# Performance work log

Hardware: AMD Instinct MI355X
Metric: run time of the kernel (lower is better)

The kernel has to match this reference:

```python
import jax, jax.numpy as jnp
import numpy as np

H = 64          # nhid
L = 2           # nlayer
N_LEFT = 100000
N_RIGHT = 100000
E = 1000000
EPS = 1e-5

PNAMES = ["nn1_w1", "nn1_b1", "nn1_w2", "nn1_b2",
          "nn2_w1", "nn2_b1", "nn2_w2", "nn2_b2",
          "l1_w", "l1_b", "l2_w", "l2_b", "l3_w", "l3_b", "l4_w", "l4_b",
          "out_w1", "out_b1", "out_w2", "out_b2"]


def _bn_relu(x):
    # BatchNorm1d (training-mode batch stats, affine=False / default-init affine) + ReLU
    m = x.mean(0, keepdims=True)
    v = jnp.mean((x - m) ** 2, axis=0, keepdims=True)  # biased var, as torch BN
    return jax.nn.relu((x - m) * jax.lax.rsqrt(v + EPS))


def _mlp2(x, w1, b1, w2, b2):
    # MLP(nin, nout, nlayer=2, with_final_activation=True): (Linear->BN->ReLU) x2
    h = _bn_relu(x @ w1 + b1)
    return _bn_relu(h @ w2 + b2)


def _lin_bn_relu(x, w, b):
    # nn.Linear -> BatchNorm1d(affine=False) -> ReLU
    return _bn_relu(x @ w + b)


def _gscatter(msg, idx, n):
    # generalized_scatter with aggregators ['add','mean','max'], concatenated
    s = jax.ops.segment_sum(msg, idx, num_segments=n)
    cnt = jax.ops.segment_sum(jnp.ones((msg.shape[0],), msg.dtype), idx, num_segments=n)[:, None]
    mean = s / jnp.maximum(cnt, 1.0)
    mx = jax.ops.segment_max(msg, idx, num_segments=n)
    mx = jnp.where(cnt > 0, mx, 0.0)  # empty segments -> 0
    return jnp.concatenate([s, mean, mx], axis=-1)  # [n, 3*d]


def _parallel_layer(xs, src, dst, nl, p):
    # nl = n_left (static). combined_batch = [0]*nl + [1]*nr (sorted), last = 1.
    nr = xs.shape[0] - nl
    x_right = xs[nl:]                                   # batch != 0
    right_info = _gscatter(x_right[dst], src, nl)       # [nl, 3H]
    x_left_new = _mlp2(xs, p["nn1_w1"], p["nn1_b1"], p["nn1_w2"], p["nn1_b2"])[:nl]
    left_info = _gscatter(x_left_new[src], dst, nr)     # [nr, 3H]
    right_info_new = _mlp2(right_info, p["nn2_w1"], p["nn2_b1"], p["nn2_w2"], p["nn2_b2"])
    right_left_info = _gscatter(right_info_new[src], dst, nr)  # [nr, 3H]
    x = _lin_bn_relu(xs, p["l1_w"], p["l1_b"])                 # [N, H//2]
    ri = _lin_bn_relu(right_info, p["l2_w"], p["l2_b"])        # [nl, H//2]
    li = _lin_bn_relu(left_info, p["l3_w"], p["l3_b"])         # [nr, H//2]
    rli = _lin_bn_relu(right_left_info, p["l4_w"], p["l4_b"])  # [nr, H//2]
    # clone-and-masked-assign patterns become static-slice concatenations
    right_full = jnp.concatenate([ri, x[nl:]], axis=0)   # rows batch!=last <- ri
    left_full = jnp.concatenate([x[:nl], li], axis=0)    # rows batch!=0    <- li
    rl_full = jnp.concatenate([x[:nl], rli], axis=0)
    h = jnp.concatenate([x, right_full, left_full, rl_full], axis=-1)  # [N, 2H]
    return _mlp2(h, p["out_w1"], p["out_b1"], p["out_w2"], p["out_b2"])


def _forward(xs, params, src, dst, n_left):
    for l in range(L):
        p = {name: params[name][l] for name in PNAMES}
        xs = xs + _parallel_layer(xs, src, dst, n_left, p)  # residual; dropout=0, eval
    return xs  # output_encoder is Identity (nin == nout)


def setup_inputs() -> dict:
    key = jax.random.key(0)
    ks = iter(jax.random.split(key, 40))
    def w(shape, s=0.1):
        return jax.random.normal(next(ks), shape, jnp.float32) * s
    inp = {
        "xs": jax.random.normal(next(ks), (N_LEFT + N_RIGHT, H), jnp.float32),
        "nn1_w1": w((L, H, H)), "nn1_b1": w((L, H)),
        "nn1_w2": w((L, H, H)), "nn1_b2": w((L, H)),
        "nn2_w1": w((L, 3 * H, H)), "nn2_b1": w((L, H)),
        "nn2_w2": w((L, H, H)), "nn2_b2": w((L, H)),
        "l1_w": w((L, H, H // 2)), "l1_b": w((L, H // 2)),
        "l2_w": w((L, 3 * H, H // 2)), "l2_b": w((L, H // 2)),
        "l3_w": w((L, 3 * H, H // 2)), "l3_b": w((L, H // 2)),
        "l4_w": w((L, 3 * H, H // 2)), "l4_b": w((L, H // 2)),
        "out_w1": w((L, 2 * H, H)), "out_b1": w((L, H)),
        "out_w2": w((L, H, H)), "out_b2": w((L, H)),
        "src": jax.random.randint(next(ks), (E,), 0, N_LEFT),
        "dst": jax.random.randint(next(ks), (E,), 0, N_RIGHT),
        "n_left": N_LEFT,
    }
    return inp


def reference(xs, nn1_w1, nn1_b1, nn1_w2, nn1_b2, nn2_w1, nn2_b1, nn2_w2, nn2_b2,
              l1_w, l1_b, l2_w, l2_b, l3_w, l3_b, l4_w, l4_b,
              out_w1, out_b1, out_w2, out_b2, src, dst, n_left):
    params = dict(zip(PNAMES, (nn1_w1, nn1_b1, nn1_w2, nn1_b2,
                               nn2_w1, nn2_b1, nn2_w2, nn2_b2,
                               l1_w, l1_b, l2_w, l2_b, l3_w, l3_b, l4_w, l4_b,
                               out_w1, out_b1, out_w2, out_b2)))
    return _forward(xs, params, src, dst, int(n_left))
```

## Files before the change

kernel.cpp:

```cpp
#include <hip/hip_runtime.h>

#define NLEFT  100000
#define NRIGHT 100000
#define NTOT   200000
#define NEDGE  1000000
#define HD     64
#define BNEPS  1e-5f

typedef __attribute__((ext_vector_type(8))) short bfrag8;
typedef __attribute__((ext_vector_type(4))) float facc4;

__device__ inline unsigned short f2bf(float f) {
  unsigned u = __float_as_uint(f);
  u = u + 0x7fffu + ((u >> 16) & 1u);
  return (unsigned short)(u >> 16);
}
__device__ inline float bf2f(unsigned short u) {
  return __uint_as_float((unsigned)u << 16);
}

#define WC_G1    0
#define WC_G2    18432
#define WC_G3    24576
#define WC_NN2W2 30720
#define WC_M2    34816
#define WC_NN1W2 40960
#define WC_OUTW1 45056
#define WC_OUTW2 53248
#define WC_PER_L 57344


__global__ __launch_bounds__(256) void init_kernel(const float* __restrict__ xs,
                                                   float* __restrict__ out,
                                                   unsigned short* __restrict__ outbf,
                                                   float* __restrict__ st, int nst,
                                                   int* __restrict__ cl, int* __restrict__ cr,
                                                   int* __restrict__ curl, int* __restrict__ curr) {
  size_t ng = (size_t)NTOT * HD / 4;
  for (size_t i = (size_t)blockIdx.x * blockDim.x + threadIdx.x; i < ng;
       i += (size_t)gridDim.x * blockDim.x) {
    float4 v = reinterpret_cast<const float4*>(xs)[i];
    reinterpret_cast<float4*>(out)[i] = v;
    ushort4 p;
    p.x = f2bf(v.x); p.y = f2bf(v.y); p.z = f2bf(v.z); p.w = f2bf(v.w);
    reinterpret_cast<ushort4*>(outbf)[i] = p;
  }
  for (int i = blockIdx.x * blockDim.x + threadIdx.x; i < NLEFT;
       i += gridDim.x * blockDim.x) {
    cl[i] = 0; curl[i] = 0; cr[i] = 0; curr[i] = 0;
    if (i < nst) st[i] = 0.f;
  }
}

__global__ __launch_bounds__(256) void count_kernel(const int* __restrict__ src,
                                                    const int* __restrict__ dst,
                                                    int* __restrict__ cl, int* __restrict__ cr) {
  for (int e = blockIdx.x * blockDim.x + threadIdx.x; e < NEDGE;
       e += gridDim.x * blockDim.x) {
    atomicAdd(&cl[src[e]], 1);
    atomicAdd(&cr[dst[e]], 1);
  }
}


__global__ __launch_bounds__(256) void wconv_kernel(const float* __restrict__ l2w,
                                                    const float* __restrict__ nn2w1,
                                                    const float* __restrict__ l4w,
                                                    const float* __restrict__ l3w,
                                                    const float* __restrict__ nn2w2,
                                                    const float* __restrict__ nn1w1,
                                                    const float* __restrict__ l1w,
                                                    const float* __restrict__ nn1w2,
                                                    const float* __restrict__ outw1,
                                                    const float* __restrict__ outw2,
                                                    unsigned short* __restrict__ dst) {
  for (int idx = blockIdx.x * 256 + threadIdx.x; idx < 2 * WC_PER_L;
       idx += gridDim.x * 256) {
    int l = idx / WC_PER_L;
    int r = idx - l * WC_PER_L;
    const float* src; int N, n, k;
    if (r < WC_G2) {
      n = r / 192; k = r - n * 192;
      if (n < 32) { src = l2w + (size_t)l * 192 * 32; N = 32; }
      else        { src = nn2w1 + (size_t)l * 192 * 64; N = 64; n -= 32; }
    } else if (r < WC_G3) {
      int rr = r - WC_G2; n = rr / 192; k = rr - n * 192;
      src = l4w + (size_t)l * 192 * 32; N = 32;
    } else if (r < WC_NN2W2) {
      int rr = r - WC_G3; n = rr / 192; k = rr - n * 192;
      src = l3w + (size_t)l * 192 * 32; N = 32;
    } else if (r < WC_M2) {
      int rr = r - WC_NN2W2; n = rr / 64; k = rr - n * 64;
      src = nn2w2 + (size_t)l * 64 * 64; N = 64;
    } else if (r < WC_NN1W2) {
      int rr = r - WC_M2; n = rr / 64; k = rr - n * 64;
      if (n < 64) { src = nn1w1 + (size_t)l * 64 * 64; N = 64; }
      else        { src = l1w + (size_t)l * 64 * 32; N = 32; n -= 64; }
    } else if (r < WC_OUTW1) {
      int rr = r - WC_NN1W2; n = rr / 64; k = rr - n * 64;
      src = nn1w2 + (size_t)l * 64 * 64; N = 64;
    } else if (r < WC_OUTW2) {
      int rr = r - WC_OUTW1; n = rr / 128; k = rr - n * 128;
      src = outw1 + (size_t)l * 128 * 64; N = 64;
    } else {
      int rr = r - WC_OUTW2; n = rr / 64; k = rr - n * 64;
      src = outw2 + (size_t)l * 64 * 64; N = 64;
    }
    dst[idx] = f2bf(src[(size_t)k * N + n]);
  }
}


__global__ __launch_bounds__(256) void scan1_kernel(const int* __restrict__ cnt, int n,
                                                    int* __restrict__ partial) {
  __shared__ int tmp[256];
  int i = blockIdx.x * 256 + threadIdx.x;
  tmp[threadIdx.x] = (i < n) ? cnt[i] : 0;
  __syncthreads();
  for (int s = 128; s > 0; s >>= 1) {
    if (threadIdx.x < s) tmp[threadIdx.x] += tmp[threadIdx.x + s];
    __syncthreads();
  }
  if (threadIdx.x == 0) partial[blockIdx.x] = tmp[0];
}

__global__ __launch_bounds__(1024) void scan2_kernel(int* __restrict__ partial, int nb) {
  __shared__ int tmp[1024];
  int t = threadIdx.x;
  int v = (t < nb) ? partial[t] : 0;
  tmp[t] = v;
  __syncthreads();
  for (int off = 1; off < 1024; off <<= 1) {
    int x = tmp[t];
    int add = (t >= off) ? tmp[t - off] : 0;
    __syncthreads();
    tmp[t] = x + add;
    __syncthreads();
  }
  if (t < nb) partial[t] = tmp[t] - v;
}

__global__ __launch_bounds__(256) void scan3_kernel(const int* __restrict__ cnt, int n,
                                                    const int* __restrict__ partial,
                                                    int* __restrict__ offs) {
  __shared__ int tmp[256];
  int t = threadIdx.x;
  int i = blockIdx.x * 256 + t;
  int v = (i < n) ? cnt[i] : 0;
  tmp[t] = v;
  __syncthreads();
  for (int off = 1; off < 256; off <<= 1) {
    int x = tmp[t];
    int add = (t >= off) ? tmp[t - off] : 0;
    __syncthreads();
    tmp[t] = x + add;
    __syncthreads();
  }
  if (i < n) offs[i] = tmp[t] - v + partial[blockIdx.x];
  if (i == 0) offs[n] = NEDGE;
}


__global__ __launch_bounds__(256) void fill_kernel(const int* __restrict__ src,
                                                   const int* __restrict__ dst,
                                                   const int* __restrict__ oL,
                                                   const int* __restrict__ oR,
                                                   int* __restrict__ curL, int* __restrict__ curR,
                                                   int* __restrict__ adjL, int* __restrict__ adjR) {
  for (int e = blockIdx.x * blockDim.x + threadIdx.x; e < NEDGE;
       e += gridDim.x * blockDim.x) {
    int s = src[e], d = dst[e];
    int p = atomicAdd(&curL[s], 1);
    adjL[oL[s] + p] = d;
    int q = atomicAdd(&curR[d], 1);
    adjR[oR[d] + q] = s;
  }
}


template <int N1, int N2, bool SRCNORM>
__global__ __launch_bounds__(512) void gmm_mfma(const unsigned short* __restrict__ mat,
                                                const int* __restrict__ offs,
                                                const int* __restrict__ adj,
                                                int nseg,
                                                const float* __restrict__ st_src, float inv_src,
                                                const unsigned short* __restrict__ Wbf,
                                                const float* __restrict__ B1,
                                                unsigned short* __restrict__ Y1,
                                                float* __restrict__ st1,
                                                const float* __restrict__ B2,
                                                unsigned short* __restrict__ Y2,
                                                float* __restrict__ st2) {
  constexpr int K    = 192;
  constexpr int LDX  = 200;
  constexpr int SEGS = 32;
  constexpr int NT   = N1 + N2;
  constexpr int CTT  = NT / 16;
  constexpr int CTW  = (CTT >= 6) ? 2 : 1;
  constexpr int NGRP = CTT / CTW;
  constexpr int NWM  = 2 * NGRP;
  __shared__ alignas(16) unsigned short xl[SEGS * LDX];
  __shared__ alignas(16) unsigned short wl[NT * LDX];
  __shared__ float bl[NT];
  __shared__ float ldsS[NT], ldsQ[NT];

  int tid = threadIdx.x;
  for (int i = tid; i < NT * 24; i += 512) {
    int n = i / 24, kk = (i - n * 24) * 8;
    *reinterpret_cast<bfrag8*>(&wl[n * LDX + kk]) =
        *reinterpret_cast<const bfrag8*>(&Wbf[n * 192 + kk]);
  }
  for (int i = tid; i < N1; i += 512) bl[i] = B1[i];
  if constexpr (N2 > 0)
    for (int i = tid; i < N2; i += 512) bl[N1 + i] = B2[i];
  if (tid < NT) { ldsS[tid] = 0.f; ldsQ[tid] = 0.f; }

  int wave = tid >> 6;
  int lane = tid & 63;
  int half = lane >> 5;
  int c0   = (lane & 31) * 2;

  float nm0 = 0.f, nm1 = 0.f, ns0 = 1.f, ns1 = 1.f;
  if (SRCNORM) {
    float m0 = st_src[c0] * inv_src, m1 = st_src[c0 + 1] * inv_src;
    float v0 = st_src[64 + c0] * inv_src - m0 * m0;
    float v1 = st_src[64 + c0 + 1] * inv_src - m1 * m1;
    nm0 = m0; nm1 = m1;
    ns0 = rsqrtf(fmaxf(v0, 0.f) + BNEPS);
    ns1 = rsqrtf(fmaxf(v1, 0.f) + BNEPS);
  }

  int lr  = lane & 15;
  int lk  = (lane >> 4) * 8;
  int lj4 = (lane >> 4) * 4;
  int rowtile = wave & 1;
  int colgrp  = wave >> 1;
  int rowbase = rowtile * 16;

  float sacc[CTW], qacc[CTW];
#pragma unroll
  for (int ct = 0; ct < CTW; ct++) { sacc[ct] = 0.f; qacc[ct] = 0.f; }

  int tiles = (nseg + SEGS - 1) / SEGS;
  for (int t = blockIdx.x; t < tiles; t += gridDim.x) {
    __syncthreads();
    int segbase = t * SEGS + wave * 4;
    for (int s = 0; s < 4; s++) {
      int seg = segbase + s;
      int row = wave * 4 + s;
      float s0 = 0.f, s1 = 0.f, m0 = -INFINITY, m1 = -INFINITY;
      int cdeg = 0;
      if (seg < nseg) {
        int b = offs[seg], e = offs[seg + 1];
        cdeg = e - b;
        for (int jb = b + half; jb < e; jb += 16) {
          unsigned pk[8];
#pragma unroll
          for (int u = 0; u < 8; u++) {
            int j = jb + 2 * u;
            pk[u] = 0;
            if (j < e) {
              int g = adj[j];
              pk[u] = *reinterpret_cast<const unsigned*>(&mat[(size_t)g * HD + c0]);
            }
          }
#pragma unroll
          for (int u = 0; u < 8; u++) {
            int j = jb + 2 * u;
            if (j < e) {
              float v0 = __uint_as_float(pk[u] << 16);
              float v1 = __uint_as_float(pk[u] & 0xffff0000u);
              if (SRCNORM) {
                v0 = fmaxf((v0 - nm0) * ns0, 0.f);
                v1 = fmaxf((v1 - nm1) * ns1, 0.f);
              }
              s0 += v0; s1 += v1;
              m0 = fmaxf(m0, v0); m1 = fmaxf(m1, v1);
            }
          }
        }
        s0 += __shfl_xor(s0, 32);
        s1 += __shfl_xor(s1, 32);
        m0 = fmaxf(m0, __shfl_xor(m0, 32));
        m1 = fmaxf(m1, __shfl_xor(m1, 32));
      }
      float inv = 1.f / fmaxf((float)cdeg, 1.f);
      if (cdeg == 0) { m0 = 0.f; m1 = 0.f; s0 = 0.f; s1 = 0.f; }
      if (half == 0) {
        unsigned sp = (unsigned)f2bf(s0) | ((unsigned)f2bf(s1) << 16);
        unsigned mp = (unsigned)f2bf(m0) | ((unsigned)f2bf(m1) << 16);
        *reinterpret_cast<unsigned*>(&xl[row * LDX + c0])       = sp;
        *reinterpret_cast<unsigned*>(&xl[row * LDX + 128 + c0]) = mp;
      } else {
        unsigned ap = (unsigned)f2bf(s0 * inv) | ((unsigned)f2bf(s1 * inv) << 16);
        *reinterpret_cast<unsigned*>(&xl[row * LDX + 64 + c0]) = ap;
      }
    }
    __syncthreads();

    if (wave < NWM) {
      facc4 acc[CTW];
#pragma unroll
      for (int ct = 0; ct < CTW; ct++) acc[ct] = (facc4){0.f, 0.f, 0.f, 0.f};
#pragma unroll
      for (int kt = 0; kt < K / 32; kt++) {
        bfrag8 a = *reinterpret_cast<const bfrag8*>(&xl[(rowbase + lr) * LDX + kt * 32 + lk]);
#pragma unroll
        for (int ct = 0; ct < CTW; ct++) {
          bfrag8 b = *reinterpret_cast<const bfrag8*>(
              &wl[((colgrp * CTW + ct) * 16 + lr) * LDX + kt * 32 + lk]);
          acc[ct] = __builtin_amdgcn_mfma_f32_16x16x32_bf16(a, b, acc[ct], 0, 0, 0);
        }
      }
#pragma unroll
      for (int ct = 0; ct < CTW; ct++) {
        int col = (colgrp * CTW + ct) * 16 + lr;
        float bias = bl[col];
#pragma unroll
        for (int j = 0; j < 4; j++) {
          int grow = t * SEGS + rowbase + lj4 + j;
          if (grow < nseg) {
            float v = acc[ct][j] + bias;
            if (col < N1) Y1[(size_t)grow * N1 + col] = f2bf(v);
            else          Y2[(size_t)grow * N2 + (col - N1)] = f2bf(v);
            sacc[ct] += v; qacc[ct] += v * v;
          }
        }
      }
    }
  }

  __syncthreads();
  if (wave < NWM) {
#pragma unroll
    for (int ct = 0; ct < CTW; ct++) {
      int col = (colgrp * CTW + ct) * 16 + lr;
      atomicAdd(&ldsS[col], sacc[ct]);
      atomicAdd(&ldsQ[col], qacc[ct]);
    }
  }
  __syncthreads();
  if (tid < NT) {
    if (tid < N1) {
      atomicAdd(&st1[tid], ldsS[tid]);
      atomicAdd(&st1[N1 + tid], ldsQ[tid]);
    } else {
      atomicAdd(&st2[tid - N1], ldsS[tid]);
      atomicAdd(&st2[N2 + (tid - N1)], ldsQ[tid]);
    }
  }
}


template <int K, int N, int ROWS, bool NIN>
__global__ __launch_bounds__(256) void mm_mfma(const unsigned short* __restrict__ X,
                                               const unsigned short* __restrict__ Wbf,
                                               const float* __restrict__ Bv,
                                               unsigned short* __restrict__ Y, int M,
                                               float* __restrict__ st_out,
                                               const float* __restrict__ st_in, float inv_m) {
  constexpr int LDX = K + 8;
  constexpr int RT  = ROWS / 64;
  constexpr int CT  = N / 16;
  constexpr int KV  = K / 8;
  __shared__ alignas(16) unsigned short xl[ROWS * LDX];
  __shared__ alignas(16) unsigned short wl[N * LDX];
  __shared__ float bl[N];
  __shared__ float nmean[K], nscal[K];
  __shared__ float ldsS[N], ldsQ[N];

  int tid = threadIdx.x;
  for (int i = tid; i < N * KV; i += 256) {
    int n = i / KV, kk = (i - n * KV) * 8;
    *reinterpret_cast<bfrag8*>(&wl[n * LDX + kk]) =
        *reinterpret_cast<const bfrag8*>(&Wbf[n * K + kk]);
  }
  for (int i = tid; i < N; i += 256) bl[i] = Bv[i];
  if (NIN) {
    for (int i = tid; i < K; i += 256) {
      float m = st_in[i] * inv_m;
      float v = st_in[K + i] * inv_m - m * m;
      nmean[i] = m;
      nscal[i] = rsqrtf(fmaxf(v, 0.f) + BNEPS);
    }
  }
  if (tid < N) { ldsS[tid] = 0.f; ldsQ[tid] = 0.f; }

  int lane = tid & 63;
  int wv   = tid >> 6;
  int lr   = lane & 15;
  int lk   = (lane >> 4) * 8;
  int lj4  = (lane >> 4) * 4;
  int rowbase = wv * (RT * 16);

  float sc[CT], sq[CT];
#pragma unroll
  for (int c = 0; c < CT; c++) { sc[c] = 0.f; sq[c] = 0.f; }

  int tiles = (M + ROWS - 1) / ROWS;
  for (int t = blockIdx.x; t < tiles; t += gridDim.x) {
    int r0 = t * ROWS;
    __syncthreads();
    for (int i = tid * 8; i < ROWS * K; i += 2048) {
      int r = i / K, c = i - r * K;
      int row = r0 + r;
      bfrag8 v = {0, 0, 0, 0, 0, 0, 0, 0};
      if (row < M) {
        v = *reinterpret_cast<const bfrag8*>(X + (size_t)row * K + c);
        if (NIN) {
#pragma unroll
          for (int j = 0; j < 8; j++) {
            float f = bf2f((unsigned short)v[j]);
            f = fmaxf((f - nmean[c + j]) * nscal[c + j], 0.f);
            v[j] = (short)f2bf(f);
          }
        }
      }
      *reinterpret_cast<bfrag8*>(&xl[r * LDX + c]) = v;
    }
    __syncthreads();

    facc4 acc[RT][CT];
#pragma unroll
    for (int rt = 0; rt < RT; rt++)
#pragma unroll
      for (int ct = 0; ct < CT; ct++) acc[rt][ct] = (facc4){0.f, 0.f, 0.f, 0.f};

#pragma unroll
    for (int kt = 0; kt < K / 32; kt++) {
      bfrag8 a[RT], b[CT];
#pragma unroll
      for (int rt = 0; rt < RT; rt++)
        a[rt] = *reinterpret_cast<const bfrag8*>(&xl[(rowbase + rt * 16 + lr) * LDX + kt * 32 + lk]);
#pragma unroll
      for (int ct = 0; ct < CT; ct++)
        b[ct] = *reinterpret_cast<const bfrag8*>(&wl[(ct * 16 + lr) * LDX + kt * 32 + lk]);
#pragma unroll
      for (int rt = 0; rt < RT; rt++)
#pragma unroll
        for (int ct = 0; ct < CT; ct++)
          acc[rt][ct] = __builtin_amdgcn_mfma_f32_16x16x32_bf16(a[rt], b[ct], acc[rt][ct], 0, 0, 0);
    }

#pragma unroll
    for (int rt = 0; rt < RT; rt++) {
#pragma unroll
      for (int ct = 0; ct < CT; ct++) {
        int col = ct * 16 + lr;
        float bcol = bl[col];
#pragma unroll
        for (int j = 0; j < 4; j++) {
          int row = r0 + rowbase + rt * 16 + lj4 + j;
          if (row < M) {
            float v = acc[rt][ct][j] + bcol;
            Y[(size_t)row * N + col] = f2bf(v);
            sc[ct] += v; sq[ct] += v * v;
          }
        }
      }
    }
  }

  __syncthreads();
#pragma unroll
  for (int ct = 0; ct < CT; ct++) {
    atomicAdd(&ldsS[ct * 16 + lr], sc[ct]);
    atomicAdd(&ldsQ[ct * 16 + lr], sq[ct]);
  }
  __syncthreads();
  if (tid < N) {
    atomicAdd(&st_out[tid], ldsS[tid]);
    atomicAdd(&st_out[N + tid], ldsQ[tid]);
  }
}


__global__ __launch_bounds__(256) void mm2_mfma(const unsigned short* __restrict__ X,
                                                const unsigned short* __restrict__ Wbf,
                                                const float* __restrict__ B1,
                                                unsigned short* __restrict__ Y1,
                                                float* __restrict__ st1,
                                                const float* __restrict__ B2,
                                                unsigned short* __restrict__ Y2,
                                                float* __restrict__ st2,
                                                int M) {
  constexpr int K = 64, N1 = 64, N2 = 32, NT = 96, ROWS = 128;
  constexpr int LDX = K + 8, RT = 2, CT = 6, KV = K / 8;
  __shared__ alignas(16) unsigned short xl[ROWS * LDX];
  __shared__ alignas(16) unsigned short wl[NT * LDX];
  __shared__ float bl[NT];
  __shared__ float ldsS[NT], ldsQ[NT];

  int tid = threadIdx.x;
  for (int i = tid; i < NT * KV; i += 256) {
    int n = i / KV, kk = (i - n * KV) * 8;
    *reinterpret_cast<bfrag8*>(&wl[n * LDX + kk]) =
        *reinterpret_cast<const bfrag8*>(&Wbf[n * K + kk]);
  }
  for (int i = tid; i < N1; i += 256) bl[i] = B1[i];
  for (int i = tid; i < N2; i += 256) bl[N1 + i] = B2[i];
  if (tid < NT) { ldsS[tid] = 0.f; ldsQ[tid] = 0.f; }

  int lane = tid & 63;
  int wv   = tid >> 6;
  int lr   = lane & 15;
  int lk   = (lane >> 4) * 8;
  int lj4  = (lane >> 4) * 4;
  int rowbase = wv * 32;

  float sc[CT], sq[CT];
#pragma unroll
  for (int c = 0; c < CT; c++) { sc[c] = 0.f; sq[c] = 0.f; }

  int tiles = (M + ROWS - 1) / ROWS;
  for (int t = blockIdx.x; t < tiles; t += gridDim.x) {
    int r0 = t * ROWS;
    __syncthreads();
    for (int i = tid * 8; i < ROWS * K; i += 2048) {
      int r = i / K, c = i - r * K;
      int row = r0 + r;
      bfrag8 v = {0, 0, 0, 0, 0, 0, 0, 0};
      if (row < M) v = *reinterpret_cast<const bfrag8*>(X + (size_t)row * K + c);
      *reinterpret_cast<bfrag8*>(&xl[r * LDX + c]) = v;
    }
    __syncthreads();

    facc4 acc[RT][CT];
#pragma unroll
    for (int rt = 0; rt < RT; rt++)
#pragma unroll
      for (int ct = 0; ct < CT; ct++) acc[rt][ct] = (facc4){0.f, 0.f, 0.f, 0.f};

#pragma unroll
    for (int kt = 0; kt < K / 32; kt++) {
      bfrag8 a[RT], b[CT];
#pragma unroll
      for (int rt = 0; rt < RT; rt++)
        a[rt] = *reinterpret_cast<const bfrag8*>(&xl[(rowbase + rt * 16 + lr) * LDX + kt * 32 + lk]);
#pragma unroll
      for (int ct = 0; ct < CT; ct++)
        b[ct] = *reinterpret_cast<const bfrag8*>(&wl[(ct * 16 + lr) * LDX + kt * 32 + lk]);
#pragma unroll
      for (int rt = 0; rt < RT; rt++)
#pragma unroll
        for (int ct = 0; ct < CT; ct++)
          acc[rt][ct] = __builtin_amdgcn_mfma_f32_16x16x32_bf16(a[rt], b[ct], acc[rt][ct], 0, 0, 0);
    }

#pragma unroll
    for (int rt = 0; rt < RT; rt++) {
#pragma unroll
      for (int ct = 0; ct < CT; ct++) {
        int col = ct * 16 + lr;
        float bcol = bl[col];
#pragma unroll
        for (int j = 0; j < 4; j++) {
          int row = r0 + rowbase + rt * 16 + lj4 + j;
          if (row < M) {
            float v = acc[rt][ct][j] + bcol;
            if (col < N1) Y1[(size_t)row * N1 + col] = f2bf(v);
            else          Y2[(size_t)row * N2 + (col - N1)] = f2bf(v);
            sc[ct] += v; sq[ct] += v * v;
          }
        }
      }
    }
  }

  __syncthreads();
#pragma unroll
  for (int ct = 0; ct < CT; ct++) {
    atomicAdd(&ldsS[ct * 16 + lr], sc[ct]);
    atomicAdd(&ldsQ[ct * 16 + lr], sq[ct]);
  }
  __syncthreads();
  if (tid < NT) {
    if (tid < N1) {
      atomicAdd(&st1[tid], ldsS[tid]);
      atomicAdd(&st1[N1 + tid], ldsQ[tid]);
    } else {
      atomicAdd(&st2[tid - N1], ldsS[tid]);
      atomicAdd(&st2[N2 + (tid - N1)], ldsQ[tid]);
    }
  }
}


__global__ __launch_bounds__(256) void mmh_mfma(const unsigned short* __restrict__ x32,
                                                const unsigned short* __restrict__ ri,
                                                const unsigned short* __restrict__ li,
                                                const unsigned short* __restrict__ rli,
                                                const float* __restrict__ stx,
                                                const float* __restrict__ stri,
                                                const float* __restrict__ stli,
                                                const float* __restrict__ strli,
                                                const unsigned short* __restrict__ Wbf,
                                                const float* __restrict__ Bv,
                                                unsigned short* __restrict__ Y,
                                                float* __restrict__ st_out) {
  constexpr int K = 128, N = 64, ROWS = 128, LDX = K + 8, RT = 2, CT = 4, KV = K / 8;
  __shared__ alignas(16) unsigned short xl[ROWS * LDX];
  __shared__ alignas(16) unsigned short wl[N * LDX];
  __shared__ float bl[N];
  __shared__ float m4[4 * 32], s4[4 * 32];
  __shared__ float ldsS[N], ldsQ[N];

  int tid = threadIdx.x;
  for (int i = tid; i < N * KV; i += 256) {
    int n = i / KV, kk = (i - n * KV) * 8;
    *reinterpret_cast<bfrag8*>(&wl[n * LDX + kk]) =
        *reinterpret_cast<const bfrag8*>(&Wbf[n * K + kk]);
  }
  for (int i = tid; i < N; i += 256) bl[i] = Bv[i];
  if (tid < 128) {
    int s = tid >> 5, c = tid & 31;
    const float* st = (s == 0) ? stx : (s == 1) ? stri : (s == 2) ? stli : strli;
    float inv = (s == 0) ? (1.f / NTOT) : (s == 1) ? (1.f / NLEFT) : (1.f / NRIGHT);
    float m = st[c] * inv;
    float v = st[32 + c] * inv - m * m;
    m4[tid] = m;
    s4[tid] = rsqrtf(fmaxf(v, 0.f) + BNEPS);
  }
  if (tid < N) { ldsS[tid] = 0.f; ldsQ[tid] = 0.f; }

  int lane = tid & 63;
  int wv   = tid >> 6;
  int lr   = lane & 15;
  int lk   = (lane >> 4) * 8;
  int lj4  = (lane >> 4) * 4;
  int rowbase = wv * 32;

  float sc[CT], sq[CT];
#pragma unroll
  for (int c = 0; c < CT; c++) { sc[c] = 0.f; sq[c] = 0.f; }

  const int M = NTOT;
  int tiles = (M + ROWS - 1) / ROWS;
  for (int t = blockIdx.x; t < tiles; t += gridDim.x) {
    int r0 = t * ROWS;
    __syncthreads();
    for (int i = tid * 8; i < ROWS * K; i += 2048) {
      int r = i / K, c = i - r * K;
      int row = r0 + r;
      bfrag8 v = {0, 0, 0, 0, 0, 0, 0, 0};
      if (row < M) {
        int cb = c >> 5, cc = c & 31;
        const unsigned short* srcp;
        int set, srow;
        if (row < NLEFT) {
          if (cb == 1) { srcp = ri;  set = 1; srow = row; }
          else         { srcp = x32; set = 0; srow = row; }
        } else {
          int rr = row - NLEFT;
          if (cb <= 1)      { srcp = x32; set = 0; srow = row; }
          else if (cb == 2) { srcp = li;  set = 2; srow = rr; }
          else              { srcp = rli; set = 3; srow = rr; }
        }
        v = *reinterpret_cast<const bfrag8*>(srcp + (size_t)srow * 32 + cc);
        const float* mm_ = &m4[set * 32 + cc];
        const float* ss_ = &s4[set * 32 + cc];
#pragma unroll
        for (int j = 0; j < 8; j++) {
          float f = bf2f((unsigned short)v[j]);
          f = fmaxf((f - mm_[j]) * ss_[j], 0.f);
          v[j] = (short)f2bf(f);
        }
      }
      *reinterpret_cast<bfrag8*>(&xl[r * LDX + c]) = v;
    }
    __syncthreads();

    facc4 acc[RT][CT];
#pragma unroll
    for (int rt = 0; rt < RT; rt++)
#pragma unroll
      for (int ct = 0; ct < CT; ct++) acc[rt][ct] = (facc4){0.f, 0.f, 0.f, 0.f};

#pragma unroll
    for (int kt = 0; kt < K / 32; kt++) {
      bfrag8 a[RT], b[CT];
#pragma unroll
      for (int rt = 0; rt < RT; rt++)
        a[rt] = *reinterpret_cast<const bfrag8*>(&xl[(rowbase + rt * 16 + lr) * LDX + kt * 32 + lk]);
#pragma unroll
      for (int ct = 0; ct < CT; ct++)
        b[ct] = *reinterpret_cast<const bfrag8*>(&wl[(ct * 16 + lr) * LDX + kt * 32 + lk]);
#pragma unroll
      for (int rt = 0; rt < RT; rt++)
#pragma unroll
        for (int ct = 0; ct < CT; ct++)
          acc[rt][ct] = __builtin_amdgcn_mfma_f32_16x16x32_bf16(a[rt], b[ct], acc[rt][ct], 0, 0, 0);
    }

#pragma unroll
    for (int rt = 0; rt < RT; rt++) {
#pragma unroll
      for (int ct = 0; ct < CT; ct++) {
        int col = ct * 16 + lr;
        float bcol = bl[col];
#pragma unroll
        for (int j = 0; j < 4; j++) {
          int row = r0 + rowbase + rt * 16 + lj4 + j;
          if (row < M) {
            float v = acc[rt][ct][j] + bcol;
            Y[(size_t)row * N + col] = f2bf(v);
            sc[ct] += v; sq[ct] += v * v;
          }
        }
      }
    }
  }

  __syncthreads();
#pragma unroll
  for (int ct = 0; ct < CT; ct++) {
    atomicAdd(&ldsS[ct * 16 + lr], sc[ct]);
    atomicAdd(&ldsQ[ct * 16 + lr], sq[ct]);
  }
  __syncthreads();
  if (tid < N) {
    atomicAdd(&st_out[tid], ldsS[tid]);
    atomicAdd(&st_out[N + tid], ldsQ[tid]);
  }
}


__global__ __launch_bounds__(256) void norm_add_kernel(const unsigned short* __restrict__ X, int M,
                                                       const float* __restrict__ st,
                                                       float* __restrict__ D,
                                                       unsigned short* __restrict__ Dbf) {
  __shared__ float mean[64], scal[64];
  if (threadIdx.x < 64) {
    float m = st[threadIdx.x] / (float)M;
    float v = st[64 + threadIdx.x] / (float)M - m * m;
    mean[threadIdx.x] = m;
    scal[threadIdx.x] = rsqrtf(fmaxf(v, 0.f) + BNEPS);
  }
  __syncthreads();
  size_t ngrp = (size_t)M * 64 / 8;
  for (size_t i = (size_t)blockIdx.x * 256 + threadIdx.x; i < ngrp;
       i += (size_t)gridDim.x * 256) {
    size_t base = i * 8;
    int c = (int)(base & 63);
    bfrag8 xv = *reinterpret_cast<const bfrag8*>(&X[base]);
    float4 d0 = *reinterpret_cast<float4*>(&D[base]);
    float4 d1 = *reinterpret_cast<float4*>(&D[base + 4]);
    float o[8];
#pragma unroll
    for (int j = 0; j < 8; j++) {
      float y = (bf2f((unsigned short)xv[j]) - mean[c + j]) * scal[c + j];
      y = y > 0.f ? y : 0.f;
      float dv = (j < 4) ? (&d0.x)[j] : (&d1.x)[j - 4];
      o[j] = dv + y;
    }
    d0 = make_float4(o[0], o[1], o[2], o[3]);
    d1 = make_float4(o[4], o[5], o[6], o[7]);
    *reinterpret_cast<float4*>(&D[base])     = d0;
    *reinterpret_cast<float4*>(&D[base + 4]) = d1;
    bfrag8 pb;
#pragma unroll
    for (int j = 0; j < 8; j++) pb[j] = (short)f2bf(o[j]);
    *reinterpret_cast<bfrag8*>(&Dbf[base]) = pb;
  }
}


static inline int tiles_of(int M, int R) { return (M + R - 1) / R; }
static inline int imin(int a, int b) { return a < b ? a : b; }

extern "C" void kernel_launch(void* const* d_in, const int* in_sizes, int n_in,
                              void* d_out, int out_size, void* d_ws, size_t ws_size,
                              hipStream_t stream) {
  const float* xs      = (const float*)d_in[0];
  const float* nn1_w1  = (const float*)d_in[1];
  const float* nn1_b1  = (const float*)d_in[2];
  const float* nn1_w2  = (const float*)d_in[3];
  const float* nn1_b2  = (const float*)d_in[4];
  const float* nn2_w1  = (const float*)d_in[5];
  const float* nn2_b1  = (const float*)d_in[6];
  const float* nn2_w2  = (const float*)d_in[7];
  const float* nn2_b2  = (const float*)d_in[8];
  const float* l1_w    = (const float*)d_in[9];
  const float* l1_b    = (const float*)d_in[10];
  const float* l2_w    = (const float*)d_in[11];
  const float* l2_b    = (const float*)d_in[12];
  const float* l3_w    = (const float*)d_in[13];
  const float* l3_b    = (const float*)d_in[14];
  const float* l4_w    = (const float*)d_in[15];
  const float* l4_b    = (const float*)d_in[16];
  const float* out_w1  = (const float*)d_in[17];
  const float* out_b1  = (const float*)d_in[18];
  const float* out_w2  = (const float*)d_in[19];
  const float* out_b2  = (const float*)d_in[20];
  const int*   src     = (const int*)d_in[21];
  const int*   dst     = (const int*)d_in[22];

  float* out = (float*)d_out;

  unsigned short* u     = (unsigned short*)d_ws;
  unsigned short* t1    = u;
  unsigned short* rin   = t1    + (size_t)NTOT * 64;
  unsigned short* x32   = rin   + (size_t)NLEFT * 64;
  unsigned short* ri32  = x32   + (size_t)NTOT * 32;
  unsigned short* li32  = ri32  + (size_t)NLEFT * 32;
  unsigned short* rli32 = li32  + (size_t)NRIGHT * 32;
  unsigned short* outbf = rli32 + (size_t)NRIGHT * 32;
  float* stats = (float*)(outbf + (size_t)NTOT * 64);
  int*   cntL  = (int*)(stats + 20 * 128);
  int*   cntR  = cntL + NLEFT;
  int*   oL    = cntR + NRIGHT;
  int*   oR    = oL + (NLEFT + 1);
  int*   curL  = oR + (NRIGHT + 1);
  int*   curR  = curL + NLEFT;
  int*   part  = curR + NRIGHT;
  int*   adjL  = part + 1024;
  int*   adjR  = adjL + NEDGE;
  unsigned short* wcvt = (unsigned short*)(adjR + NEDGE);

  dim3 B(256);
  const int NB1 = (NLEFT + 255) / 256;
  const float invL = 1.f / NLEFT, invT = 1.f / NTOT;
  const int tilesL = tiles_of(NLEFT, 32);
  const int GD = imin(tilesL, 768);
  const int GS = imin(tilesL, 1536);

  init_kernel<<<2048, B, 0, stream>>>(xs, out, outbf, stats, 20 * 128, cntL, cntR, curL, curR);
  wconv_kernel<<<448, B, 0, stream>>>(l2_w, nn2_w1, l4_w, l3_w, nn2_w2, nn1_w1, l1_w,
                                      nn1_w2, out_w1, out_w2, wcvt);
  count_kernel<<<2048, B, 0, stream>>>(src, dst, cntL, cntR);
  scan1_kernel<<<NB1, B, 0, stream>>>(cntL, NLEFT, part);
  scan2_kernel<<<1, 1024, 0, stream>>>(part, NB1);
  scan3_kernel<<<NB1, B, 0, stream>>>(cntL, NLEFT, part, oL);
  scan1_kernel<<<NB1, B, 0, stream>>>(cntR, NRIGHT, part);
  scan2_kernel<<<1, 1024, 0, stream>>>(part, NB1);
  scan3_kernel<<<NB1, B, 0, stream>>>(cntR, NRIGHT, part, oR);
  fill_kernel<<<2048, B, 0, stream>>>(src, dst, oL, oR, curL, curR, adjL, adjR);

  for (int l = 0; l < 2; l++) {
    const float* p_nn1_b1 = nn1_b1 + (size_t)l * 64;
    const float* p_nn1_b2 = nn1_b2 + (size_t)l * 64;
    const float* p_nn2_b1 = nn2_b1 + (size_t)l * 64;
    const float* p_nn2_b2 = nn2_b2 + (size_t)l * 64;
    const float* p_l1_b   = l1_b + (size_t)l * 32;
    const float* p_l2_b   = l2_b + (size_t)l * 32;
    const float* p_l3_b   = l3_b + (size_t)l * 32;
    const float* p_l4_b   = l4_b + (size_t)l * 32;
    const float* p_out_b1 = out_b1 + (size_t)l * 64;
    const float* p_out_b2 = out_b2 + (size_t)l * 64;
    const unsigned short* wc = wcvt + (size_t)l * WC_PER_L;

    float* S = stats + (size_t)l * 10 * 128;
    auto ST = [&](int s) { return S + (size_t)s * 128; };

    gmm_mfma<32, 64, false><<<GD, 512, 0, stream>>>(
        outbf + (size_t)NLEFT * 64, oL, adjL, NLEFT, nullptr, 0.f,
        wc + WC_G1, p_l2_b, ri32, ST(0), p_nn2_b1, rin, ST(1));
    mm_mfma<64, 64, 128, true><<<tiles_of(NLEFT, 128), B, 0, stream>>>(
        rin, wc + WC_NN2W2, p_nn2_b2, rin, NLEFT, ST(2), ST(1), invL);
    gmm_mfma<32, 0, true><<<GS, 512, 0, stream>>>(
        rin, oR, adjR, NRIGHT, ST(2), invL,
        wc + WC_G2, p_l4_b, rli32, ST(3), nullptr, nullptr, nullptr);
    mm2_mfma<<<tiles_of(NTOT, 128), B, 0, stream>>>(
        outbf, wc + WC_M2, p_nn1_b1, t1, ST(4), p_l1_b, x32, ST(7), NTOT);
    mm_mfma<64, 64, 128, true><<<tiles_of(NTOT, 128), B, 0, stream>>>(
        t1, wc + WC_NN1W2, p_nn1_b2, t1, NTOT, ST(5), ST(4), invT);
    gmm_mfma<32, 0, true><<<GS, 512, 0, stream>>>(
        t1, oR, adjR, NRIGHT, ST(5), invT,
        wc + WC_G3, p_l3_b, li32, ST(6), nullptr, nullptr, nullptr);
    mmh_mfma<<<tiles_of(NTOT, 128), B, 0, stream>>>(
        x32, ri32, li32, rli32, ST(7), ST(0), ST(6), ST(3),
        wc + WC_OUTW1, p_out_b1, t1, ST(8));
    mm_mfma<64, 64, 128, true><<<tiles_of(NTOT, 128), B, 0, stream>>>(
        t1, wc + WC_OUTW2, p_out_b2, t1, NTOT, ST(9), ST(8), invT);
    norm_add_kernel<<<2048, B, 0, stream>>>(t1, NTOT, ST(9), out, outbf);
  }
}
```

Measured before the change: 1.290 ms.

## Partition CSR fill into key-range passes and stage adjacency tiles in LDS

The CSR fill kernel is split into eight launches, each handling one side (left or right) and a quarter of the key range. The aim is to keep the atomic counters and adjacency writes inside a smaller working set, at the cost of rereading the full edge list several times. The gather GEMM kernel also copies each 32-segment tile's adjacency indices into shared memory when they fit within 448 entries, so per-edge index loads hit LDS instead of global memory. This adds an extra block barrier per tile and uses more shared memory.

```diff
diff --git a/kernel.cpp b/kernel.cpp
--- a/kernel.cpp
+++ b/kernel.cpp
@@ -6,6 +6,7 @@
 #define NEDGE  1000000
 #define HD     64
 #define BNEPS  1e-5f
+#define ADJ_CAP 448
 
 typedef __attribute__((ext_vector_type(8))) short bfrag8;
 typedef __attribute__((ext_vector_type(4))) float facc4;
@@ -161,19 +162,19 @@
 }
 
 
-__global__ __launch_bounds__(256) void fill_kernel(const int* __restrict__ src,
-                                                   const int* __restrict__ dst,
-                                                   const int* __restrict__ oL,
-                                                   const int* __restrict__ oR,
-                                                   int* __restrict__ curL, int* __restrict__ curR,
-                                                   int* __restrict__ adjL, int* __restrict__ adjR) {
+__global__ __launch_bounds__(256) void fillp_kernel(const int* __restrict__ key,
+                                                    const int* __restrict__ val,
+                                                    const int* __restrict__ offs,
+                                                    int* __restrict__ cur,
+                                                    int* __restrict__ adjout,
+                                                    int lo, int hi) {
   for (int e = blockIdx.x * blockDim.x + threadIdx.x; e < NEDGE;
        e += gridDim.x * blockDim.x) {
-    int s = src[e], d = dst[e];
-    int p = atomicAdd(&curL[s], 1);
-    adjL[oL[s] + p] = d;
-    int q = atomicAdd(&curR[d], 1);
-    adjR[oR[d] + q] = s;
+    int k = key[e];
+    if (k >= lo && k < hi) {
+      int p = atomicAdd(&cur[k], 1);
+      adjout[offs[k] + p] = val[e];
+    }
   }
 }
 
@@ -203,6 +204,7 @@
   __shared__ alignas(16) unsigned short wl[NT * LDX];
   __shared__ float bl[NT];
   __shared__ float ldsS[NT], ldsQ[NT];
+  __shared__ int adjs[ADJ_CAP];
 
   int tid = threadIdx.x;
   for (int i = tid; i < NT * 24; i += 512) {
@@ -244,7 +246,16 @@
   int tiles = (nseg + SEGS - 1) / SEGS;
   for (int t = blockIdx.x; t < tiles; t += gridDim.x) {
     __syncthreads();
-    int segbase = t * SEGS + wave * 4;
+    int seg_lo = t * SEGS;
+    int seg_hi = seg_lo + SEGS; if (seg_hi > nseg) seg_hi = nseg;
+    int abase = offs[seg_lo];
+    int acnt  = offs[seg_hi] - abase;
+    bool lds_adj = (acnt <= ADJ_CAP);
+    if (lds_adj)
+      for (int i = tid; i < acnt; i += 512) adjs[i] = adj[abase + i];
+    __syncthreads();
+
+    int segbase = seg_lo + wave * 4;
     for (int s = 0; s < 4; s++) {
       int seg = segbase + s;
       int row = wave * 4 + s;
@@ -260,7 +271,7 @@
             int j = jb + 2 * u;
             pk[u] = 0;
             if (j < e) {
-              int g = adj[j];
+              int g = lds_adj ? adjs[j - abase] : adj[j];
               pk[u] = *reinterpret_cast<const unsigned*>(&mat[(size_t)g * HD + c0]);
             }
           }
@@ -834,7 +845,11 @@
   scan1_kernel<<<NB1, B, 0, stream>>>(cntR, NRIGHT, part);
   scan2_kernel<<<1, 1024, 0, stream>>>(part, NB1);
   scan3_kernel<<<NB1, B, 0, stream>>>(cntR, NRIGHT, part, oR);
-  fill_kernel<<<2048, B, 0, stream>>>(src, dst, oL, oR, curL, curR, adjL, adjR);
+  for (int p = 0; p < 4; p++) {
+    int lo = p * (NLEFT / 4), hi = (p + 1) * (NLEFT / 4);
+    fillp_kernel<<<2048, B, 0, stream>>>(src, dst, oL, curL, adjL, lo, hi);
+    fillp_kernel<<<2048, B, 0, stream>>>(dst, src, oR, curR, adjR, lo, hi);
+  }
 
   for (int l = 0; l < 2; l++) {
     const float* p_nn1_b1 = nn1_b1 + (size_t)l * 64;
```

Result: slower. 1.362 ms (+5.6%).

## Fuse the two right-side gather-aggregate-matmul passes into one kernel

Applied to the files above, without the earlier changes.

Replaces two separate gmm_mfma launches over the same right-side adjacency (one for right_info_new, one for x_left_new) with a single gmm2_mfma kernel. It walks each segment's edge list once, gathering both source matrices per edge. It applies each matrix's BN+ReLU, builds sum/mean/max for both, and runs both 32-column projections with one weight tile that holds the contiguous G2/G3 weights. This removes a duplicate read of offsets and adjacency indices plus a launch. The costs are higher register and LDS pressure per block and a smaller grid (GD instead of GS).

```diff
diff --git a/kernel.cpp b/kernel.cpp
--- a/kernel.cpp
+++ b/kernel.cpp
@@ -352,6 +352,177 @@
 }
 
 
+__global__ __launch_bounds__(512) void gmm2_mfma(const unsigned short* __restrict__ matA,
+                                                 const float* __restrict__ stA, float invA,
+                                                 const unsigned short* __restrict__ matB,
+                                                 const float* __restrict__ stB, float invB,
+                                                 const int* __restrict__ offs,
+                                                 const int* __restrict__ adj,
+                                                 int nseg,
+                                                 const unsigned short* __restrict__ Wbf,
+                                                 const float* __restrict__ BA,
+                                                 const float* __restrict__ BB,
+                                                 unsigned short* __restrict__ YA,
+                                                 float* __restrict__ st1,
+                                                 unsigned short* __restrict__ YB,
+                                                 float* __restrict__ st2) {
+  constexpr int K = 192, LDX = 200, SEGS = 32;
+  __shared__ alignas(16) unsigned short xlA[SEGS * LDX];
+  __shared__ alignas(16) unsigned short xlB[SEGS * LDX];
+  __shared__ alignas(16) unsigned short wl[64 * LDX];
+  __shared__ float bl[64];
+  __shared__ float ldsS[64], ldsQ[64];
+
+  int tid = threadIdx.x;
+  for (int i = tid; i < 64 * 24; i += 512) {
+    int n = i / 24, kk = (i - n * 24) * 8;
+    *reinterpret_cast<bfrag8*>(&wl[n * LDX + kk]) =
+        *reinterpret_cast<const bfrag8*>(&Wbf[n * 192 + kk]);
+  }
+  if (tid < 32) bl[tid] = BA[tid];
+  else if (tid < 64) bl[tid] = BB[tid - 32];
+  if (tid < 64) { ldsS[tid] = 0.f; ldsQ[tid] = 0.f; }
+
+  int wave = tid >> 6;
+  int lane = tid & 63;
+  int half = lane >> 5;
+  int c0   = (lane & 31) * 2;
+
+  float nmA0, nmA1, nsA0, nsA1, nmB0, nmB1, nsB0, nsB1;
+  {
+    float m0 = stA[c0] * invA, m1 = stA[c0 + 1] * invA;
+    float v0 = stA[64 + c0] * invA - m0 * m0;
+    float v1 = stA[64 + c0 + 1] * invA - m1 * m1;
+    nmA0 = m0; nmA1 = m1;
+    nsA0 = rsqrtf(fmaxf(v0, 0.f) + BNEPS);
+    nsA1 = rsqrtf(fmaxf(v1, 0.f) + BNEPS);
+    m0 = stB[c0] * invB; m1 = stB[c0 + 1] * invB;
+    v0 = stB[64 + c0] * invB - m0 * m0;
+    v1 = stB[64 + c0 + 1] * invB - m1 * m1;
+    nmB0 = m0; nmB1 = m1;
+    nsB0 = rsqrtf(fmaxf(v0, 0.f) + BNEPS);
+    nsB1 = rsqrtf(fmaxf(v1, 0.f) + BNEPS);
+  }
+
+  int lr  = lane & 15;
+  int lk  = (lane >> 4) * 8;
+  int lj4 = (lane >> 4) * 4;
+  int grp     = wave >> 2;
+  int rowtile = wave & 1;
+  int ctile   = (wave >> 1) & 1;
+  int rowbase = rowtile * 16;
+
+  float sacc = 0.f, qacc = 0.f;
+
+  int tiles = (nseg + SEGS - 1) / SEGS;
+  for (int t = blockIdx.x; t < tiles; t += gridDim.x) {
+    __syncthreads();
+    int segbase = t * SEGS + wave * 4;
+    for (int s = 0; s < 4; s++) {
+      int seg = segbase + s;
+      int row = wave * 4 + s;
+      float sA0 = 0.f, sA1 = 0.f, mA0 = -INFINITY, mA1 = -INFINITY;
+      float sB0 = 0.f, sB1 = 0.f, mB0 = -INFINITY, mB1 = -INFINITY;
+      int cdeg = 0;
+      if (seg < nseg) {
+        int b = offs[seg], e = offs[seg + 1];
+        cdeg = e - b;
+        for (int jb = b + half; jb < e; jb += 16) {
+          unsigned pkA[8], pkB[8];
+#pragma unroll
+          for (int u = 0; u < 8; u++) {
+            int j = jb + 2 * u;
+            pkA[u] = 0; pkB[u] = 0;
+            if (j < e) {
+              int g = adj[j];
+              pkA[u] = *reinterpret_cast<const unsigned*>(&matA[(size_t)g * HD + c0]);
+              pkB[u] = *reinterpret_cast<const unsigned*>(&matB[(size_t)g * HD + c0]);
+            }
+          }
+#pragma unroll
+          for (int u = 0; u < 8; u++) {
+            int j = jb + 2 * u;
+            if (j < e) {
+              float a0 = fmaxf((__uint_as_float(pkA[u] << 16) - nmA0) * nsA0, 0.f);
+              float a1 = fmaxf((__uint_as_float(pkA[u] & 0xffff0000u) - nmA1) * nsA1, 0.f);
+              float b0 = fmaxf((__uint_as_float(pkB[u] << 16) - nmB0) * nsB0, 0.f);
+              float b1 = fmaxf((__uint_as_float(pkB[u] & 0xffff0000u) - nmB1) * nsB1, 0.f);
+              sA0 += a0; sA1 += a1; mA0 = fmaxf(mA0, a0); mA1 = fmaxf(mA1, a1);
+              sB0 += b0; sB1 += b1; mB0 = fmaxf(mB0, b0); mB1 = fmaxf(mB1, b1);
+            }
+          }
+        }
+        sA0 += __shfl_xor(sA0, 32);
+        sA1 += __shfl_xor(sA1, 32);
+        mA0 = fmaxf(mA0, __shfl_xor(mA0, 32));
+        mA1 = fmaxf(mA1, __shfl_xor(mA1, 32));
+        sB0 += __shfl_xor(sB0, 32);
+        sB1 += __shfl_xor(sB1, 32);
+        mB0 = fmaxf(mB0, __shfl_xor(mB0, 32));
+        mB1 = fmaxf(mB1, __shfl_xor(mB1, 32));
+      }
+      float inv = 1.f / fmaxf((float)cdeg, 1.f);
+      if (cdeg == 0) { mA0 = 0.f; mA1 = 0.f; mB0 = 0.f; mB1 = 0.f;
+                       sA0 = 0.f; sA1 = 0.f; sB0 = 0.f; sB1 = 0.f; }
+      if (half == 0) {
+        *reinterpret_cast<unsigned*>(&xlA[row * LDX + c0]) =
+            (unsigned)f2bf(sA0) | ((unsigned)f2bf(sA1) << 16);
+        *reinterpret_cast<unsigned*>(&xlA[row * LDX + 128 + c0]) =
+            (unsigned)f2bf(mA0) | ((unsigned)f2bf(mA1) << 16);
+        *reinterpret_cast<unsigned*>(&xlB[row * LDX + c0]) =
+            (unsigned)f2bf(sB0) | ((unsigned)f2bf(sB1) << 16);
+        *reinterpret_cast<unsigned*>(&xlB[row * LDX + 128 + c0]) =
+            (unsigned)f2bf(mB0) | ((unsigned)f2bf(mB1) << 16);
+      } else {
+        *reinterpret_cast<unsigned*>(&xlA[row * LDX + 64 + c0]) =
+            (unsigned)f2bf(sA0 * inv) | ((unsigned)f2bf(sA1 * inv) << 16);
+        *reinterpret_cast<unsigned*>(&xlB[row * LDX + 64 + c0]) =
+            (unsigned)f2bf(sB0 * inv) | ((unsigned)f2bf(sB1 * inv) << 16);
+      }
+    }
+    __syncthreads();
+
+    {
+      const unsigned short* xl = grp ? xlB : xlA;
+      facc4 acc = (facc4){0.f, 0.f, 0.f, 0.f};
+#pragma unroll
+      for (int kt = 0; kt < K / 32; kt++) {
+        bfrag8 a = *reinterpret_cast<const bfrag8*>(&xl[(rowbase + lr) * LDX + kt * 32 + lk]);
+        bfrag8 b = *reinterpret_cast<const bfrag8*>(
+            &wl[(grp * 32 + ctile * 16 + lr) * LDX + kt * 32 + lk]);
+        acc = __builtin_amdgcn_mfma_f32_16x16x32_bf16(a, b, acc, 0, 0, 0);
+      }
+      int col = ctile * 16 + lr;
+      float bias = bl[grp * 32 + col];
+      unsigned short* Y = grp ? YB : YA;
+#pragma unroll
+      for (int j = 0; j < 4; j++) {
+        int grow = t * SEGS + rowbase + lj4 + j;
+        if (grow < nseg) {
+          float v = acc[j] + bias;
+          Y[(size_t)grow * 32 + col] = f2bf(v);
+          sacc += v; qacc += v * v;
+        }
+      }
+    }
+  }
+
+  __syncthreads();
+  atomicAdd(&ldsS[grp * 32 + ctile * 16 + lr], sacc);
+  atomicAdd(&ldsQ[grp * 32 + ctile * 16 + lr], qacc);
+  __syncthreads();
+  if (tid < 64) {
+    if (tid < 32) {
+      atomicAdd(&st1[tid], ldsS[tid]);
+      atomicAdd(&st1[32 + tid], ldsQ[tid]);
+    } else {
+      atomicAdd(&st2[tid - 32], ldsS[tid]);
+      atomicAdd(&st2[32 + (tid - 32)], ldsQ[tid]);
+    }
+  }
+}
+
+
 template <int K, int N, int ROWS, bool NIN>
 __global__ __launch_bounds__(256) void mm_mfma(const unsigned short* __restrict__ X,
                                                const unsigned short* __restrict__ Wbf,
@@ -822,7 +993,6 @@
   const float invL = 1.f / NLEFT, invT = 1.f / NTOT;
   const int tilesL = tiles_of(NLEFT, 32);
   const int GD = imin(tilesL, 768);
-  const int GS = imin(tilesL, 1536);
 
   init_kernel<<<2048, B, 0, stream>>>(xs, out, outbf, stats, 20 * 128, cntL, cntR, curL, curR);
   wconv_kernel<<<448, B, 0, stream>>>(l2_w, nn2_w1, l4_w, l3_w, nn2_w2, nn1_w1, l1_w,
@@ -857,16 +1027,13 @@
         wc + WC_G1, p_l2_b, ri32, ST(0), p_nn2_b1, rin, ST(1));
     mm_mfma<64, 64, 128, true><<<tiles_of(NLEFT, 128), B, 0, stream>>>(
         rin, wc + WC_NN2W2, p_nn2_b2, rin, NLEFT, ST(2), ST(1), invL);
-    gmm_mfma<32, 0, true><<<GS, 512, 0, stream>>>(
-        rin, oR, adjR, NRIGHT, ST(2), invL,
-        wc + WC_G2, p_l4_b, rli32, ST(3), nullptr, nullptr, nullptr);
     mm2_mfma<<<tiles_of(NTOT, 128), B, 0, stream>>>(
         outbf, wc + WC_M2, p_nn1_b1, t1, ST(4), p_l1_b, x32, ST(7), NTOT);
     mm_mfma<64, 64, 128, true><<<tiles_of(NTOT, 128), B, 0, stream>>>(
         t1, wc + WC_NN1W2, p_nn1_b2, t1, NTOT, ST(5), ST(4), invT);
-    gmm_mfma<32, 0, true><<<GS, 512, 0, stream>>>(
-        t1, oR, adjR, NRIGHT, ST(5), invT,
-        wc + WC_G3, p_l3_b, li32, ST(6), nullptr, nullptr, nullptr);
+    gmm2_mfma<<<GD, 512, 0, stream>>>(
+        rin, ST(2), invL, t1, ST(5), invT, oR, adjR, NRIGHT,
+        wc + WC_G2, p_l4_b, p_l3_b, rli32, ST(3), li32, ST(6));
     mmh_mfma<<<tiles_of(NTOT, 128), B, 0, stream>>>(
         x32, ri32, li32, rli32, ST(7), ST(0), ST(6), ST(3),
         wc + WC_OUTW1, p_out_b1, t1, ST(8));
```

New measurement: 1.148 ms (median of 2 runs). -11.0%, faster.
